# Kernel tuning notes

Hardware: AMD Instinct MI355X
Metric: run time of the kernel (lower is better)

The kernel has to match this reference:

```python
import jax, jax.numpy as jnp
import numpy as np

B, T, E, H = 2, 2048, 1024, 16
D = E // H  # head_dim = 64


def setup_inputs() -> dict:
    key = jax.random.key(0)
    kx, kq, kk, kv, ko = jax.random.split(key, 5)
    x = jax.random.normal(kx, (B, T, E), dtype=jnp.float32)
    # nn.Parameter(torch.randn(...)) -> standard normal params
    Wq = jax.random.normal(kq, (H, E, D), dtype=jnp.float32)
    Wk = jax.random.normal(kk, (H, E, D), dtype=jnp.float32)
    Wv = jax.random.normal(kv, (H, E, D), dtype=jnp.float32)
    # nn.Linear(E, E, bias=False): weight [out, in], y = a @ Wo.T
    Wo = jax.random.normal(ko, (E, E), dtype=jnp.float32) * (1.0 / np.sqrt(E))
    # boolean mask: True positions are filled with -inf (causal: strict upper tri)
    mask = jnp.triu(jnp.ones((T, T), dtype=bool), k=1)
    return {"x": x, "mask": mask, "Wq": Wq, "Wk": Wk, "Wv": Wv, "Wo": Wo}


def reference(x, mask, Wq, Wk, Wv, Wo):
    # x: [b, t, e]; Wq/Wk/Wv: [h, e, i]
    q = jnp.einsum('hei,bte->hbti', Wq, x)
    k = jnp.einsum('hei,bte->hbti', Wk, x)
    v = jnp.einsum('hei,bte->hbti', Wv, x)
    # NOTE: original scales by sqrt(seq_len) (x.shape[1]), not sqrt(head_dim)
    scale = x.shape[1] ** 0.5
    fit = jnp.einsum('hbti,hbTi->hbtT', q, k) / scale  # [h, b, t, T]
    fit = jnp.where(mask, -jnp.inf, fit)
    p = jax.nn.softmax(fit, axis=-1)
    att = jnp.einsum('hbtT,hbTi->hbti', p, v)          # [h, b, t, i]
    # rearrange 'h b t i -> b t (h i)'
    b, t = att.shape[1], att.shape[2]
    att = jnp.transpose(att, (1, 2, 0, 3)).reshape(b, t, -1)
    return att @ Wo.T
```

## Files before the change

kernel.cpp:

```cpp
#include <hip/hip_runtime.h>
#include <hip/hip_fp8.h>
#include <stdint.h>

constexpr float INV_SCALE = 0.022097086912079608f;
constexpr float LOG2E = 1.4426950408889634f;
constexpr float QSC = INV_SCALE * LOG2E;

typedef __attribute__((ext_vector_type(8))) short bfrag;
typedef __attribute__((ext_vector_type(4))) float facc;
typedef __attribute__((ext_vector_type(4))) unsigned short us4;

#define MFMA(a, b, c) __builtin_amdgcn_mfma_f32_16x16x32_bf16((a), (b), (c), 0, 0, 0)
#define EXP2(x) __builtin_amdgcn_exp2f(x)

__device__ __forceinline__ unsigned short f2bh(float f) {
    union { float f; unsigned int u; } cv; cv.f = f;
    unsigned int u = cv.u;
    u += 0x7FFFu + ((u >> 16) & 1u);
    return (unsigned short)(u >> 16);
}
__device__ __forceinline__ float bh2f(unsigned short h) {
    union { unsigned int u; float f; } cv; cv.u = ((unsigned int)h) << 16;
    return cv.f;
}
__device__ __forceinline__ void gl_lds16(const unsigned short* g, unsigned short* lds) {
    __builtin_amdgcn_global_load_lds(
        (const __attribute__((address_space(1))) unsigned int*)g,
        (__attribute__((address_space(3))) unsigned int*)lds, 16, 0, 0);
}
__device__ __forceinline__ bfrag f8frag(uint2 raw) {
    union { uint2 u; unsigned char b[8]; } cv; cv.u = raw;
    bfrag r;
    #pragma unroll
    for (int j = 0; j < 8; ++j) {
        const __hip_fp8_e4m3* t = reinterpret_cast<const __hip_fp8_e4m3*>(&cv.b[j]);
        r[j] = (short)f2bh((float)(*t) * 0.00390625f);
    }
    return r;
}
template<int CTRL>
__device__ __forceinline__ float dppmax(float v) {
    int s = __builtin_amdgcn_update_dpp(0, __builtin_bit_cast(int, v), CTRL, 0xF, 0xF, true);
    return fmaxf(v, __builtin_bit_cast(float, s));
}
__device__ __forceinline__ float rowmax16(float v) {
    v = dppmax<0xB1>(v);
    v = dppmax<0x4E>(v);
    v = dppmax<0x141>(v);
    v = dppmax<0x140>(v);
    return v;
}

__global__ __launch_bounds__(256) void prep_all(
    const float* __restrict__ x, const float* __restrict__ Wo,
    const float* __restrict__ Wq, const float* __restrict__ Wk, const float* __restrict__ Wv,
    unsigned short* __restrict__ xh, unsigned short* __restrict__ xl,
    unsigned short* __restrict__ WoB,
    unsigned short* __restrict__ WqTh, unsigned short* __restrict__ WqTl,
    unsigned short* __restrict__ WkTh, unsigned short* __restrict__ WkTl,
    unsigned short* __restrict__ WvT)
{
    __shared__ float tile[64][65];
    const int tid = threadIdx.x;
    const int bx = blockIdx.x;
    if (bx < 768) {
        const int et = bx & 15, h = (bx >> 4) & 15, m = bx >> 8;
        const float* W = (m == 0) ? Wq : (m == 1) ? Wk : Wv;
        #pragma unroll
        for (int rep = 0; rep < 4; ++rep) {
            int idx = rep * 256 + tid;
            int e = idx >> 4, i4 = (idx & 15) * 4;
            facc v = *(const facc*)&W[(size_t)h * 65536 + (size_t)(et * 64 + e) * 64 + i4];
            tile[e][i4] = v.x; tile[e][i4 + 1] = v.y; tile[e][i4 + 2] = v.z; tile[e][i4 + 3] = v.w;
        }
        __syncthreads();
        unsigned short* Oh = (m == 0) ? WqTh : (m == 1) ? WkTh : WvT;
        unsigned short* Ol = (m == 0) ? WqTl : WkTl;
        #pragma unroll
        for (int rep = 0; rep < 4; ++rep) {
            int idx = rep * 256 + tid;
            int i = idx >> 4, e4 = (idx & 15) * 4;
            us4 hv, lv;
            #pragma unroll
            for (int j = 0; j < 4; ++j) {
                float f = tile[e4 + j][i];
                unsigned short hb = f2bh(f);
                hv[j] = hb;
                lv[j] = f2bh(f - bh2f(hb));
            }
            size_t o = (size_t)(h * 64 + i) * 1024 + et * 64 + e4;
            *(us4*)&Oh[o] = hv;
            if (m < 2) *(us4*)&Ol[o] = lv;
        }
    } else if (bx < 1792) {
        int idx = (bx - 768) * 256 + tid;
        facc v = *(const facc*)&Wo[(size_t)idx * 4];
        us4 o;
        #pragma unroll
        for (int j = 0; j < 4; ++j) o[j] = f2bh(v[j]);
        *(us4*)&WoB[(size_t)idx * 4] = o;
    } else {
        int idx = (bx - 1792) * 256 + tid;
        facc v = *(const facc*)&x[(size_t)idx * 4];
        us4 hv, lv;
        #pragma unroll
        for (int j = 0; j < 4; ++j) {
            unsigned short hb = f2bh(v[j]);
            hv[j] = hb;
            lv[j] = f2bh(v[j] - bh2f(hb));
        }
        *(us4*)&xh[(size_t)idx * 4] = hv;
        *(us4*)&xl[(size_t)idx * 4] = lv;
    }
}

__global__ __launch_bounds__(256, 2) void qkv_fused(
    const unsigned short* __restrict__ xh, const unsigned short* __restrict__ xl,
    const unsigned short* __restrict__ WqTh, const unsigned short* __restrict__ WqTl,
    const unsigned short* __restrict__ WkTh, const unsigned short* __restrict__ WkTl,
    const unsigned short* __restrict__ WvT,
    unsigned short* __restrict__ qh, unsigned char* __restrict__ ql8,
    unsigned short* __restrict__ kh, unsigned short* __restrict__ kl,
    unsigned short* __restrict__ vT)
{
    extern __shared__ unsigned short sm[];
    unsigned short* Ab = sm;
    unsigned short* Qb = sm + 16384;
    unsigned short* Kb = sm + 24576;
    unsigned short* Vb = sm + 32768;
    const int tid = threadIdx.x;
    const int w = tid >> 6, l = tid & 63;
    const int wm = w >> 1, wn = w & 1;
    const int ct = blockIdx.x, rt = blockIdx.y;

    const int lc = (l & 7) ^ (l >> 3);
    const int krel = (lc & 3) * 8;
    const unsigned short* Axp = (lc < 4) ? xh : xl;
    const unsigned short* Qp  = (lc < 4) ? WqTh : WqTl;
    const unsigned short* Kp  = (lc < 4) ? WkTh : WkTl;
    const int lcv = (l & 3) ^ ((l >> 3) & 3);

    facc accq[4][2], acck[4][2], accv[4][2];
    #pragma unroll
    for (int m = 0; m < 4; ++m)
        #pragma unroll
        for (int n = 0; n < 2; ++n) {
            accq[m][n] = (facc)(0.0f); acck[m][n] = (facc)(0.0f); accv[m][n] = (facc)(0.0f);
        }

    auto stageV = [&](int buf, int e0) {
        int row = w * 16 + (l >> 2);
        gl_lds16(&WvT[(size_t)(ct * 64 + row) * 1024 + e0 + lcv * 8],
                 &Vb[buf * 2048 + w * 512]);
    };

    {
        #pragma unroll
        for (int i = 0; i < 4; ++i) {
            int slice = w * 4 + i;
            int row = slice * 8 + (l >> 3);
            gl_lds16(&Axp[(size_t)(rt * 128 + row) * 1024 + krel], &Ab[slice * 512]);
        }
        #pragma unroll
        for (int i = 0; i < 2; ++i) {
            int slice = w * 2 + i;
            int row = slice * 8 + (l >> 3);
            size_t sb = (size_t)(ct * 64 + row) * 1024 + krel;
            gl_lds16(&Qp[sb], &Qb[slice * 512]);
            gl_lds16(&Kp[sb], &Kb[slice * 512]);
        }
        stageV(0, 0);
    }
    asm volatile("s_waitcnt vmcnt(0)" ::: "memory");
    __builtin_amdgcn_s_barrier();

    for (int t = 0; t < 32; ++t) {
        __builtin_amdgcn_s_barrier();
        __builtin_amdgcn_sched_barrier(0);
        if (t < 31) {
            int buf = (t + 1) & 1, e0 = (t + 1) * 32;
            #pragma unroll
            for (int i = 0; i < 4; ++i) {
                int slice = w * 4 + i;
                int row = slice * 8 + (l >> 3);
                gl_lds16(&Axp[(size_t)(rt * 128 + row) * 1024 + e0 + krel],
                         &Ab[buf * 8192 + slice * 512]);
            }
            #pragma unroll
            for (int i = 0; i < 2; ++i) {
                int slice = w * 2 + i;
                int row = slice * 8 + (l >> 3);
                size_t sb = (size_t)(ct * 64 + row) * 1024 + e0 + krel;
                gl_lds16(&Qp[sb], &Qb[buf * 4096 + slice * 512]);
                gl_lds16(&Kp[sb], &Kb[buf * 4096 + slice * 512]);
            }
            stageV(buf, e0);
        }
        __builtin_amdgcn_sched_barrier(0);
        if (t < 31) asm volatile("s_waitcnt vmcnt(9)" ::: "memory");
        else        asm volatile("s_waitcnt vmcnt(0)" ::: "memory");
        __builtin_amdgcn_sched_barrier(0);
        __builtin_amdgcn_s_barrier();
        __builtin_amdgcn_sched_barrier(0);

        const unsigned short* Ac = &Ab[(t & 1) * 8192];
        const unsigned short* Qc = &Qb[(t & 1) * 4096];
        const unsigned short* Kc = &Kb[(t & 1) * 4096];
        const unsigned short* Vc = &Vb[(t & 1) * 2048];
        const int ca = (l >> 4) ^ (l & 7);
        const int cb = ca ^ 4;

        bfrag afh[4], afl[4];
        #pragma unroll
        for (int m = 0; m < 4; ++m) {
            int row = wm * 64 + m * 16 + (l & 15);
            afh[m] = *(const bfrag*)&Ac[row * 64 + ca * 8];
            afl[m] = *(const bfrag*)&Ac[row * 64 + cb * 8];
        }
        #pragma unroll
        for (int n = 0; n < 2; ++n) {
            int nr = wn * 32 + n * 16 + (l & 15);
            int cv = (l >> 4) ^ ((nr >> 1) & 3);
            bfrag bv = *(const bfrag*)&Vc[nr * 32 + cv * 8];
            #pragma unroll
            for (int m = 0; m < 4; ++m) accv[m][n] = MFMA(afh[m], bv, accv[m][n]);
        }
        #pragma unroll
        for (int n = 0; n < 2; ++n) {
            int nr = wn * 32 + n * 16 + (l & 15);
            bfrag bh = *(const bfrag*)&Qc[nr * 64 + ca * 8];
            bfrag bl = *(const bfrag*)&Qc[nr * 64 + cb * 8];
            #pragma unroll
            for (int m = 0; m < 4; ++m) {
                accq[m][n] = MFMA(afh[m], bh, accq[m][n]);
                accq[m][n] = MFMA(afh[m], bl, accq[m][n]);
                accq[m][n] = MFMA(afl[m], bh, accq[m][n]);
            }
        }
        #pragma unroll
        for (int n = 0; n < 2; ++n) {
            int nr = wn * 32 + n * 16 + (l & 15);
            bfrag bh = *(const bfrag*)&Kc[nr * 64 + ca * 8];
            bfrag bl = *(const bfrag*)&Kc[nr * 64 + cb * 8];
            #pragma unroll
            for (int m = 0; m < 4; ++m) {
                acck[m][n] = MFMA(afh[m], bh, acck[m][n]);
                acck[m][n] = MFMA(afh[m], bl, acck[m][n]);
                acck[m][n] = MFMA(afl[m], bh, acck[m][n]);
            }
        }
    }

    #pragma unroll
    for (int m = 0; m < 4; ++m)
        #pragma unroll
        for (int r = 0; r < 4; ++r) {
            int row = rt * 128 + wm * 64 + m * 16 + (l >> 4) * 4 + r;
            #pragma unroll
            for (int n = 0; n < 2; ++n) {
                int col = ct * 64 + wn * 32 + n * 16 + (l & 15);
                float fq = accq[m][n][r] * QSC;
                unsigned short hb = f2bh(fq);
                qh[(size_t)row * 1024 + col] = hb;
                __hip_fp8_e4m3 e((fq - bh2f(hb)) * 256.0f);
                ql8[(size_t)row * 1024 + col] = *reinterpret_cast<unsigned char*>(&e);
                float fk = acck[m][n][r];
                unsigned short kb = f2bh(fk);
                kh[(size_t)row * 1024 + col] = kb;
                kl[(size_t)row * 1024 + col] = f2bh(fk - bh2f(kb));
            }
        }
    #pragma unroll
    for (int m = 0; m < 4; ++m) {
        int t0g = rt * 128 + wm * 64 + m * 16 + (l >> 4) * 4;
        int b_ = t0g >> 11, t0 = t0g & 2047;
        #pragma unroll
        for (int n = 0; n < 2; ++n) {
            int col = ct * 64 + wn * 32 + n * 16 + (l & 15);
            int h_ = col >> 6, d = col & 63;
            us4 pk;
            #pragma unroll
            for (int r = 0; r < 4; ++r) pk[r] = f2bh(accv[m][n][r]);
            *(us4*)&vT[((size_t)((h_ * 2 + b_) * 64 + d)) * 2048 + t0] = pk;
        }
    }
}

__device__ __forceinline__ void stage_k(
    const unsigned short* __restrict__ kh, const unsigned short* __restrict__ kl,
    unsigned short* Khb, unsigned short* Klb, int w, int l, int b, int h, int kt)
{
    #pragma unroll
    for (int i = 0; i < 2; ++i) {
        int pbase = (w * 2 + i) * 1024;
        int p = pbase + l * 16;
        int row = p >> 7, slot = (p >> 4) & 7;
        int chunk = slot ^ (row & 7);
        size_t srcK = (size_t)(b * 2048 + kt * 64 + row) * 1024 + h * 64 + chunk * 8;
        gl_lds16(&kh[srcK], &Khb[pbase >> 1]);
        gl_lds16(&kl[srcK], &Klb[pbase >> 1]);
    }
}
__device__ __forceinline__ void stage_v(
    const unsigned short* __restrict__ vT, unsigned short* Vtb,
    int w, int l, int b, int h, int kt)
{
    #pragma unroll
    for (int i = 0; i < 2; ++i) {
        int pbase = (w * 2 + i) * 1024;
        int p = pbase + l * 16;
        int row = p >> 7, slot = (p >> 4) & 7;
        int chunk = slot ^ (row & 7);
        size_t srcV = ((size_t)(h * 2 + b) * 64 + row) * 2048 + (size_t)kt * 64 + chunk * 8;
        gl_lds16(&vT[srcV], &Vtb[pbase >> 1]);
    }
}

__global__ __launch_bounds__(256, 3) void attn_mfma(
    const unsigned short* __restrict__ qh, const unsigned char* __restrict__ ql8,
    const unsigned short* __restrict__ kh, const unsigned short* __restrict__ kl,
    const unsigned short* __restrict__ vT, unsigned short* __restrict__ att)
{
    __shared__ unsigned short Kh[2][4096], Kl[2][4096], Vt[4096], Pl[4096];
    const int tid = threadIdx.x, w = tid >> 6, l = tid & 63;
    const int dd = blockIdx.y * 32 + blockIdx.x;
    const int xcd = dd & 7, sl = dd >> 3;
    const int qt = 31 - (sl >> 2);
    const int hb = xcd * 4 + (sl & 3);
    const int h = hb >> 1, b = hb & 1;

    bfrag ones;
    #pragma unroll
    for (int j = 0; j < 8; ++j) ones[j] = (short)0x3F80;

    bfrag qfh[2], qfl[2];
    {
        const int qrow = qt * 64 + w * 16 + (l & 15);
        const size_t qoff = (size_t)(b * 2048 + qrow) * 1024 + h * 64 + (l >> 4) * 8;
        qfh[0] = *(const bfrag*)&qh[qoff];
        qfh[1] = *(const bfrag*)&qh[qoff + 32];
        qfl[0] = f8frag(*(const uint2*)&ql8[qoff]);
        qfl[1] = f8frag(*(const uint2*)&ql8[qoff + 32]);
    }

    facc O[4], Osum;
    float mrow[4];
    #pragma unroll
    for (int f = 0; f < 4; ++f) O[f] = (facc)(0.0f);
    Osum = (facc)(0.0f);
    #pragma unroll
    for (int r = 0; r < 4; ++r) mrow[r] = -1e30f;

    stage_k(kh, kl, Kh[0], Kl[0], w, l, b, h, 0);
    for (int kt = 0; kt <= qt; ++kt) {
        const int cur = kt & 1;
        __syncthreads();
        stage_v(vT, Vt, w, l, b, h, kt);
        if (kt < qt)
            stage_k(kh, kl, Kh[cur ^ 1], Kl[cur ^ 1], w, l, b, h, kt + 1);
        __builtin_amdgcn_sched_barrier(0);
        __builtin_amdgcn_s_barrier();
        __builtin_amdgcn_sched_barrier(0);

        facc S[4];
        #pragma unroll
        for (int f = 0; f < 4; ++f) S[f] = (facc)(0.0f);
        __builtin_amdgcn_s_setprio(1);
        #pragma unroll
        for (int s = 0; s < 2; ++s) {
            #pragma unroll
            for (int f = 0; f < 4; ++f) {
                int key = f * 16 + (l & 15);
                int ch = (s * 4 + (l >> 4)) ^ (key & 7);
                bfrag kbh = *(const bfrag*)&Kh[cur][key * 64 + ch * 8];
                bfrag kbl = *(const bfrag*)&Kl[cur][key * 64 + ch * 8];
                S[f] = MFMA(qfh[s], kbh, S[f]);
                S[f] = MFMA(qfh[s], kbl, S[f]);
                S[f] = MFMA(qfl[s], kbh, S[f]);
            }
        }
        __builtin_amdgcn_s_setprio(0);
        if (kt == qt) {
            #pragma unroll
            for (int f = 0; f < 4; ++f) {
                int keyl = f * 16 + (l & 15);
                #pragma unroll
                for (int r = 0; r < 4; ++r) {
                    int qls = w * 16 + (l >> 4) * 4 + r;
                    if (keyl > qls) S[f][r] = -1e30f;
                }
            }
        }
        float mx[4];
        float dmax = -3.0e38f;
        #pragma unroll
        for (int r = 0; r < 4; ++r) {
            float m0 = fmaxf(fmaxf(S[0][r], S[1][r]), fmaxf(S[2][r], S[3][r]));
            m0 = rowmax16(m0);
            mx[r] = m0;
            dmax = fmaxf(dmax, m0 - mrow[r]);
        }
        if (!__all(dmax <= 8.0f)) {
            #pragma unroll
            for (int r = 0; r < 4; ++r) {
                float mn = fmaxf(mrow[r], mx[r]);
                float fac = EXP2(mrow[r] - mn);
                mrow[r] = mn;
                O[0][r] *= fac; O[1][r] *= fac; O[2][r] *= fac; O[3][r] *= fac;
                Osum[r] *= fac;
            }
        }
        #pragma unroll
        for (int r = 0; r < 4; ++r)
            #pragma unroll
            for (int f = 0; f < 4; ++f) S[f][r] = EXP2(S[f][r] - mrow[r]);
        #pragma unroll
        for (int f = 0; f < 4; ++f) {
            int key = f * 16 + (l & 15);
            #pragma unroll
            for (int r = 0; r < 4; ++r) {
                int qr = w * 16 + (l >> 4) * 4 + r;
                Pl[qr * 64 + (((key >> 3) ^ (qr & 7)) * 8) + (key & 7)] = f2bh(S[f][r]);
            }
        }
        __builtin_amdgcn_sched_barrier(0);
        if (kt < qt) asm volatile("s_waitcnt vmcnt(4)" ::: "memory");
        else         asm volatile("s_waitcnt vmcnt(0)" ::: "memory");
        __builtin_amdgcn_sched_barrier(0);
        __builtin_amdgcn_s_barrier();
        __builtin_amdgcn_sched_barrier(0);
        __builtin_amdgcn_s_setprio(1);
        #pragma unroll
        for (int s = 0; s < 2; ++s) {
            int qa = w * 16 + (l & 15);
            int cha = (s * 4 + (l >> 4)) ^ (qa & 7);
            bfrag pa = *(const bfrag*)&Pl[qa * 64 + cha * 8];
            Osum = MFMA(pa, ones, Osum);
            #pragma unroll
            for (int f = 0; f < 4; ++f) {
                int d = f * 16 + (l & 15);
                int chv = (s * 4 + (l >> 4)) ^ (d & 7);
                bfrag vb = *(const bfrag*)&Vt[d * 64 + chv * 8];
                O[f] = MFMA(pa, vb, O[f]);
            }
        }
        __builtin_amdgcn_s_setprio(0);
    }

    #pragma unroll
    for (int f = 0; f < 4; ++f) {
        int d = h * 64 + f * 16 + (l & 15);
        #pragma unroll
        for (int r = 0; r < 4; ++r) {
            int t = qt * 64 + w * 16 + (l >> 4) * 4 + r;
            att[(size_t)(b * 2048 + t) * 1024 + d] = f2bh(O[f][r] / Osum[r]);
        }
    }
}

__global__ __launch_bounds__(256, 2) void outproj(
    const unsigned short* __restrict__ att, const unsigned short* __restrict__ WoB,
    float* __restrict__ out)
{
    __shared__ unsigned short Ab[2][128 * 64], Bb[2][128 * 64];
    const int tid = threadIdx.x, w = tid >> 6, l = tid & 63;
    const int wm = w >> 1, wn = w & 1;
    const int rt = blockIdx.x, ct = blockIdx.y;

    const int lc = (l & 7) ^ (l >> 3);
    facc acc[4][4];
    #pragma unroll
    for (int i = 0; i < 4; ++i)
        #pragma unroll
        for (int j = 0; j < 4; ++j) acc[i][j] = (facc)(0.0f);

    auto stage = [&](int buf, int e0) {
        #pragma unroll
        for (int i = 0; i < 4; ++i) {
            int slice = w * 4 + i;
            int row = slice * 8 + (l >> 3);
            gl_lds16(&att[(size_t)(rt * 128 + row) * 1024 + e0 + lc * 8], &Ab[buf][slice * 512]);
            gl_lds16(&WoB[(size_t)(ct * 128 + row) * 1024 + e0 + lc * 8], &Bb[buf][slice * 512]);
        }
    };

    stage(0, 0);
    int cur = 0;
    for (int t = 0; t < 16; ++t) {
        __syncthreads();
        if (t < 15) stage(cur ^ 1, (t + 1) * 64);
        __builtin_amdgcn_sched_barrier(0);
        __builtin_amdgcn_s_barrier();
        __builtin_amdgcn_sched_barrier(0);
        #pragma unroll
        for (int s = 0; s < 2; ++s) {
            const int slot = (s * 4 + (l >> 4)) ^ (l & 7);
            bfrag af[4], bf_[4];
            #pragma unroll
            for (int m = 0; m < 4; ++m)
                af[m] = *(const bfrag*)&Ab[cur][(wm * 64 + m * 16 + (l & 15)) * 64 + slot * 8];
            #pragma unroll
            for (int n = 0; n < 4; ++n)
                bf_[n] = *(const bfrag*)&Bb[cur][(wn * 64 + n * 16 + (l & 15)) * 64 + slot * 8];
            #pragma unroll
            for (int m = 0; m < 4; ++m)
                #pragma unroll
                for (int n = 0; n < 4; ++n)
                    acc[m][n] = MFMA(af[m], bf_[n], acc[m][n]);
        }
        cur ^= 1;
    }
    #pragma unroll
    for (int m = 0; m < 4; ++m)
        #pragma unroll
        for (int r = 0; r < 4; ++r) {
            int row = rt * 128 + wm * 64 + m * 16 + (l >> 4) * 4 + r;
            #pragma unroll
            for (int n = 0; n < 4; ++n) {
                int col = ct * 128 + wn * 64 + n * 16 + (l & 15);
                out[(size_t)row * 1024 + col] = acc[m][n][r];
            }
        }
}

extern "C" void kernel_launch(void* const* d_in, const int* in_sizes, int n_in,
                              void* d_out, int out_size, void* d_ws, size_t ws_size,
                              hipStream_t stream) {
    const float* x  = (const float*)d_in[0];
    const float* Wq = (const float*)d_in[2];
    const float* Wk = (const float*)d_in[3];
    const float* Wv = (const float*)d_in[4];
    const float* Wo = (const float*)d_in[5];

    uint8_t* wsb = (uint8_t*)d_ws;
    const size_t MB = 1024 * 1024;
    unsigned short* WqTh = (unsigned short*)(wsb + 0 * MB);
    unsigned short* WqTl = (unsigned short*)(wsb + 2 * MB);
    unsigned short* WkTh = (unsigned short*)(wsb + 4 * MB);
    unsigned short* WkTl = (unsigned short*)(wsb + 6 * MB);
    unsigned short* WvT  = (unsigned short*)(wsb + 8 * MB);
    unsigned short* qh   = (unsigned short*)(wsb + 10 * MB);
    unsigned char*  ql8  = (unsigned char*)(wsb + 18 * MB);
    unsigned short* kh   = (unsigned short*)(wsb + 22 * MB);
    unsigned short* kl   = (unsigned short*)(wsb + 30 * MB);
    unsigned short* vT   = (unsigned short*)(wsb + 38 * MB);
    unsigned short* att  = (unsigned short*)(wsb + 46 * MB);
    unsigned short* xh   = (unsigned short*)(wsb + 46 * MB);
    unsigned short* WoB  = (unsigned short*)(wsb + 54 * MB);
    unsigned short* xl   = (unsigned short*)(wsb + 56 * MB);

    hipFuncSetAttribute((const void*)qkv_fused,
                        hipFuncAttributeMaxDynamicSharedMemorySize, 73728);

    prep_all<<<dim3(5888), 256, 0, stream>>>(x, Wo, Wq, Wk, Wv, xh, xl, WoB,
                                             WqTh, WqTl, WkTh, WkTl, WvT);
    qkv_fused<<<dim3(16, 32), 256, 73728, stream>>>(xh, xl, WqTh, WqTl, WkTh, WkTl, WvT,
                                                    qh, ql8, kh, kl, vT);
    attn_mfma<<<dim3(32, 32), 256, 0, stream>>>(qh, ql8, kh, kl, vT, att);
    outproj<<<dim3(32, 8), 256, 0, stream>>>(att, WoB, (float*)d_out);
}
```

Measured before the change: 152.9 us.

## Single-buffer weight tiles in qkv_fused to cut LDS and raise occupancy

Moves qkv_fused from dynamic to static shared memory and double-buffers only the activation tile, so the Q, K and V weight tiles each get a single buffer. The weight tiles are now loaded at the start of each k-step and waited on before compute, while only the next activation tile is prefetched. Launch bounds go from 2 to 3 blocks per CU to exploit the smaller LDS footprint. The cost is that weight-load latency is no longer hidden behind compute, and the tighter register budget may cause spills. With only 512 blocks, the extra occupancy may add little.

```diff
diff --git a/kernel.cpp b/kernel.cpp
--- a/kernel.cpp
+++ b/kernel.cpp
@@ -114,7 +114,7 @@
     }
 }
 
-__global__ __launch_bounds__(256, 2) void qkv_fused(
+__global__ __launch_bounds__(256, 3) void qkv_fused(
     const unsigned short* __restrict__ xh, const unsigned short* __restrict__ xl,
     const unsigned short* __restrict__ WqTh, const unsigned short* __restrict__ WqTl,
     const unsigned short* __restrict__ WkTh, const unsigned short* __restrict__ WkTl,
@@ -123,11 +123,10 @@
     unsigned short* __restrict__ kh, unsigned short* __restrict__ kl,
     unsigned short* __restrict__ vT)
 {
-    extern __shared__ unsigned short sm[];
-    unsigned short* Ab = sm;
-    unsigned short* Qb = sm + 16384;
-    unsigned short* Kb = sm + 24576;
-    unsigned short* Vb = sm + 32768;
+    __shared__ unsigned short Ab[2][8192];
+    __shared__ unsigned short Qb[4096];
+    __shared__ unsigned short Kb[4096];
+    __shared__ unsigned short Vb[2048];
     const int tid = threadIdx.x;
     const int w = tid >> 6, l = tid & 63;
     const int wm = w >> 1, wn = w & 1;
@@ -148,65 +147,43 @@
             accq[m][n] = (facc)(0.0f); acck[m][n] = (facc)(0.0f); accv[m][n] = (facc)(0.0f);
         }
 
-    auto stageV = [&](int buf, int e0) {
-        int row = w * 16 + (l >> 2);
-        gl_lds16(&WvT[(size_t)(ct * 64 + row) * 1024 + e0 + lcv * 8],
-                 &Vb[buf * 2048 + w * 512]);
-    };
-
-    {
+    auto stageA = [&](int buf, int e0) {
         #pragma unroll
         for (int i = 0; i < 4; ++i) {
             int slice = w * 4 + i;
             int row = slice * 8 + (l >> 3);
-            gl_lds16(&Axp[(size_t)(rt * 128 + row) * 1024 + krel], &Ab[slice * 512]);
-        }
+            gl_lds16(&Axp[(size_t)(rt * 128 + row) * 1024 + e0 + krel],
+                     &Ab[buf][slice * 512]);
+        }
+    };
+    auto stageQKV = [&](int e0) {
         #pragma unroll
         for (int i = 0; i < 2; ++i) {
             int slice = w * 2 + i;
             int row = slice * 8 + (l >> 3);
-            size_t sb = (size_t)(ct * 64 + row) * 1024 + krel;
+            size_t sb = (size_t)(ct * 64 + row) * 1024 + e0 + krel;
             gl_lds16(&Qp[sb], &Qb[slice * 512]);
             gl_lds16(&Kp[sb], &Kb[slice * 512]);
         }
-        stageV(0, 0);
-    }
-    asm volatile("s_waitcnt vmcnt(0)" ::: "memory");
-    __builtin_amdgcn_s_barrier();
+        int row = w * 16 + (l >> 2);
+        gl_lds16(&WvT[(size_t)(ct * 64 + row) * 1024 + e0 + lcv * 8], &Vb[w * 512]);
+    };
+
+    stageA(0, 0);
 
     for (int t = 0; t < 32; ++t) {
+        __syncthreads();
+        stageQKV(t * 32);
+        __builtin_amdgcn_sched_barrier(0);
+        if (t < 31) stageA((t + 1) & 1, (t + 1) * 32);
+        __builtin_amdgcn_sched_barrier(0);
+        if (t < 31) asm volatile("s_waitcnt vmcnt(4)" ::: "memory");
+        else        asm volatile("s_waitcnt vmcnt(0)" ::: "memory");
+        __builtin_amdgcn_sched_barrier(0);
         __builtin_amdgcn_s_barrier();
         __builtin_amdgcn_sched_barrier(0);
-        if (t < 31) {
-            int buf = (t + 1) & 1, e0 = (t + 1) * 32;
-            #pragma unroll
-            for (int i = 0; i < 4; ++i) {
-                int slice = w * 4 + i;
-                int row = slice * 8 + (l >> 3);
-                gl_lds16(&Axp[(size_t)(rt * 128 + row) * 1024 + e0 + krel],
-                         &Ab[buf * 8192 + slice * 512]);
-            }
-            #pragma unroll
-            for (int i = 0; i < 2; ++i) {
-                int slice = w * 2 + i;
-                int row = slice * 8 + (l >> 3);
-                size_t sb = (size_t)(ct * 64 + row) * 1024 + e0 + krel;
-                gl_lds16(&Qp[sb], &Qb[buf * 4096 + slice * 512]);
-                gl_lds16(&Kp[sb], &Kb[buf * 4096 + slice * 512]);
-            }
-            stageV(buf, e0);
-        }
-        __builtin_amdgcn_sched_barrier(0);
-        if (t < 31) asm volatile("s_waitcnt vmcnt(9)" ::: "memory");
-        else        asm volatile("s_waitcnt vmcnt(0)" ::: "memory");
-        __builtin_amdgcn_sched_barrier(0);
-        __builtin_amdgcn_s_barrier();
-        __builtin_amdgcn_sched_barrier(0);
-
-        const unsigned short* Ac = &Ab[(t & 1) * 8192];
-        const unsigned short* Qc = &Qb[(t & 1) * 4096];
-        const unsigned short* Kc = &Kb[(t & 1) * 4096];
-        const unsigned short* Vc = &Vb[(t & 1) * 2048];
+
+        const unsigned short* Ac = Ab[t & 1];
         const int ca = (l >> 4) ^ (l & 7);
         const int cb = ca ^ 4;
 
@@ -221,15 +198,15 @@
         for (int n = 0; n < 2; ++n) {
             int nr = wn * 32 + n * 16 + (l & 15);
             int cv = (l >> 4) ^ ((nr >> 1) & 3);
-            bfrag bv = *(const bfrag*)&Vc[nr * 32 + cv * 8];
+            bfrag bv = *(const bfrag*)&Vb[nr * 32 + cv * 8];
             #pragma unroll
             for (int m = 0; m < 4; ++m) accv[m][n] = MFMA(afh[m], bv, accv[m][n]);
         }
         #pragma unroll
         for (int n = 0; n < 2; ++n) {
             int nr = wn * 32 + n * 16 + (l & 15);
-            bfrag bh = *(const bfrag*)&Qc[nr * 64 + ca * 8];
-            bfrag bl = *(const bfrag*)&Qc[nr * 64 + cb * 8];
+            bfrag bh = *(const bfrag*)&Qb[nr * 64 + ca * 8];
+            bfrag bl = *(const bfrag*)&Qb[nr * 64 + cb * 8];
             #pragma unroll
             for (int m = 0; m < 4; ++m) {
                 accq[m][n] = MFMA(afh[m], bh, accq[m][n]);
@@ -240,8 +217,8 @@
         #pragma unroll
         for (int n = 0; n < 2; ++n) {
             int nr = wn * 32 + n * 16 + (l & 15);
-            bfrag bh = *(const bfrag*)&Kc[nr * 64 + ca * 8];
-            bfrag bl = *(const bfrag*)&Kc[nr * 64 + cb * 8];
+            bfrag bh = *(const bfrag*)&Kb[nr * 64 + ca * 8];
+            bfrag bl = *(const bfrag*)&Kb[nr * 64 + cb * 8];
             #pragma unroll
             for (int m = 0; m < 4; ++m) {
                 acck[m][n] = MFMA(afh[m], bh, acck[m][n]);
@@ -549,13 +526,10 @@
     unsigned short* WoB  = (unsigned short*)(wsb + 54 * MB);
     unsigned short* xl   = (unsigned short*)(wsb + 56 * MB);
 
-    hipFuncSetAttribute((const void*)qkv_fused,
-                        hipFuncAttributeMaxDynamicSharedMemorySize, 73728);
-
     prep_all<<<dim3(5888), 256, 0, stream>>>(x, Wo, Wq, Wk, Wv, xh, xl, WoB,
                                              WqTh, WqTl, WkTh, WkTl, WvT);
-    qkv_fused<<<dim3(16, 32), 256, 73728, stream>>>(xh, xl, WqTh, WqTl, WkTh, WkTl, WvT,
-                                                    qh, ql8, kh, kl, vT);
+    qkv_fused<<<dim3(16, 32), 256, 0, stream>>>(xh, xl, WqTh, WqTl, WkTh, WkTl, WvT,
+                                                qh, ql8, kh, kl, vT);
     attn_mfma<<<dim3(32, 32), 256, 0, stream>>>(qh, ql8, kh, kl, vT, att);
     outproj<<<dim3(32, 8), 256, 0, stream>>>(att, WoB, (float*)d_out);
 }
```

Measured after the change: 150.6 us. About the same (-1.5%).
